# Performance work log

Measured on AMD Instinct MI355X. Metric: run time of the kernel, lower is better.

Reference implementation:

```python
import jax, jax.numpy as jnp
import numpy as np

D_MODEL = 1024
H = 16
D_K = D_MODEL // H
D_FF = 4096
EPS = 1e-6
NEG = -1e9


def setup_inputs() -> dict:
    key = jax.random.key(0)
    ks = jax.random.split(key, 8)
    B, S = 2, 2048
    src = jax.random.normal(ks[0], (B, S, D_MODEL), dtype=jnp.float32)
    src_mask = jnp.ones((B, 1, 1, S), dtype=jnp.int32)
    sc = 1.0 / np.sqrt(D_MODEL)
    wq = jax.random.normal(ks[1], (D_MODEL, D_MODEL), jnp.float32) * sc
    wk = jax.random.normal(ks[2], (D_MODEL, D_MODEL), jnp.float32) * sc
    wv = jax.random.normal(ks[3], (D_MODEL, D_MODEL), jnp.float32) * sc
    wo = jax.random.normal(ks[4], (D_MODEL, D_MODEL), jnp.float32) * sc
    w1 = jax.random.normal(ks[5], (D_FF, D_MODEL), jnp.float32) * sc
    b1 = jnp.zeros((D_FF,), jnp.float32)
    w2 = jax.random.normal(ks[6], (D_MODEL, D_FF), jnp.float32) * (1.0 / np.sqrt(D_FF))
    b2 = jnp.zeros((D_MODEL,), jnp.float32)
    a1 = jnp.ones((1,), jnp.float32)
    be1 = jnp.zeros((1,), jnp.float32)
    a2 = jnp.ones((1,), jnp.float32)
    be2 = jnp.zeros((1,), jnp.float32)
    return dict(src=src, src_mask=src_mask, wq=wq, wk=wk, wv=wv, wo=wo,
                w1=w1, b1=b1, w2=w2, b2=b2, a1=a1, be1=be1, a2=a2, be2=be2)


def layer_norm(x, alpha, bias):
    # torch: mean + unbiased std (ddof=1), eps added to std
    mean = jnp.mean(x, axis=-1, keepdims=True)
    std = jnp.sqrt(jnp.var(x, axis=-1, keepdims=True, ddof=1))
    return alpha * (x - mean) / (std + EPS) + bias


def mha(x, mask, wq, wk, wv, wo):
    B, S, _ = x.shape
    def split(t):  # [B,S,D] -> [B,H,S,D_K]
        return t.reshape(B, S, H, D_K).transpose(0, 2, 1, 3)
    q = split(x @ wq.T)
    k = split(x @ wk.T)
    v = split(x @ wv.T)
    scores = jnp.einsum('bhqd,bhkd->bhqk', q, k) / np.sqrt(D_K)
    scores = jnp.where(mask == 0, NEG, scores)
    attn = jax.nn.softmax(scores, axis=-1)
    out = jnp.einsum('bhqk,bhkd->bhqd', attn, v)
    out = out.transpose(0, 2, 1, 3).reshape(B, S, D_MODEL)
    return out @ wo.T


def reference(src, src_mask, wq, wk, wv, wo, w1, b1, w2, b2, a1, be1, a2, be2):
    x = layer_norm(src, a1, be1)
    src = src + mha(x, src_mask, wq, wk, wv, wo)
    x = layer_norm(src, a2, be2)
    ff = jax.nn.relu(x @ w1.T + b1) @ w2.T + b2
    return src + ff
```

## Files before the change

kernel.cpp:

```cpp
#include <hip/hip_runtime.h>
#include <hip/hip_bf16.h>

typedef unsigned short u16;
typedef unsigned int u32;
typedef float floatx4 __attribute__((ext_vector_type(4)));
typedef __bf16 bf16x8 __attribute__((ext_vector_type(8)));
typedef u16 ushort4v __attribute__((ext_vector_type(4)));
typedef u16 ushort8v __attribute__((ext_vector_type(8)));
typedef u32 u32x2 __attribute__((ext_vector_type(2)));

#define DEVI static __device__ __forceinline__

DEVI u16 f2bf(float f) {
    u32 u = __builtin_bit_cast(u32, f);
    u += 0x7fffu + ((u >> 16) & 1u);
    return (u16)(u >> 16);
}
DEVI float bf2f(u16 h) { return __builtin_bit_cast(float, (u32)h << 16); }

DEVI float fexp2(float x) { return __builtin_amdgcn_exp2f(x); }

DEVI u32 cvtpk_bf16(float lo, float hi) {
    u32 r;
    asm("v_cvt_pk_bf16_f32 %0, %1, %2" : "=v"(r) : "v"(lo), "v"(hi));
    return r;
}

DEVI void async_cp16(const u16* g, u16* l) {
    __builtin_amdgcn_global_load_lds((const __attribute__((address_space(1))) u32*)g,
                                     (__attribute__((address_space(3))) u32*)l, 16, 0, 0);
}

template<int N> DEVI void wait_vmcnt() {
    if constexpr (N == 0)      asm volatile("s_waitcnt vmcnt(0)" ::: "memory");
    else if constexpr (N == 2) asm volatile("s_waitcnt vmcnt(2)" ::: "memory");
    else if constexpr (N == 3) asm volatile("s_waitcnt vmcnt(3)" ::: "memory");
    else if constexpr (N == 4) asm volatile("s_waitcnt vmcnt(4)" ::: "memory");
    else if constexpr (N == 6) asm volatile("s_waitcnt vmcnt(6)" ::: "memory");
    else static_assert(N == 0, "add vmcnt case");
}

#define PH_BAR() asm volatile("s_barrier" ::: "memory")

template<int BM, int BN, int RW, int CW, bool QKV3, int NSPLIT, bool XSWZ,
         bool BIAS, bool RELU, bool RESID, bool OBF16, bool VTW>
__global__ __launch_bounds__(256) void gemm_nt(
    const u16* __restrict__ A,
    const u16* __restrict__ W0, const u16* __restrict__ W1, const u16* __restrict__ W2,
    const float* __restrict__ bias, const float* __restrict__ resid,
    void* __restrict__ o0, void* __restrict__ o1, void* __restrict__ o2,
    void* __restrict__ o3, int K, int lda, int Nper, int NX)
{
    static_assert(RW * CW == 4, "4 waves");
    constexpr int WM = BM / RW, WN = BN / CW;
    constexpr int MI = WM / 16, NI = WN / 16;
    constexpr int LPT = BM / 64 + BN / 64;
    constexpr int ASZ = 3 * BM * 32;
    constexpr int BSZ = 3 * BN * 32;
    __shared__ __align__(16) u16 smem[ASZ + BSZ];
    u16* Asm = smem;
    u16* Bsm = smem + ASZ;
    const int tid = threadIdx.x;
    const int w = tid >> 6, lane = tid & 63;
    const int q = lane >> 4, ml = lane & 15;
    const int wr = w / CW, wc = w % CW;
    int bx = blockIdx.x, by = blockIdx.y;
    if (XSWZ) {
        const int gx = gridDim.x, gy = gridDim.y;
        int L = by * gx + bx;
        int xcd = L & 7, s = L >> 3;
        int mb = gy >> 3;
        by = xcd * mb + s % mb;
        bx = s / mb;
    }
    const int m0 = by * BM;
    size_t kbase = 0;
    const u16* W = W0;
    void* outp = o0;
    if (NSPLIT > 1) {
        int part = bx / NX; bx -= part * NX; kbase = (size_t)part * K;
        outp = (part == 0) ? o0 : (part == 1 ? o1 : (part == 2 ? o2 : o3));
    }
    int n0 = bx * BN;
    bool vwrite = false;
    if (QKV3) {
        int sel = n0 / Nper;
        n0 -= sel * Nper;
        W = (sel == 0) ? W0 : (sel == 1 ? W1 : W2);
        outp = (sel == 0) ? o0 : (sel == 1 ? o1 : o2);
        if (VTW) vwrite = (sel == 2);
    }

    auto stage = [&](int buf, int kt) {
#pragma unroll
        for (int p = 0; p < BM / 64; ++p) {
            int g = p * 256 + tid;
            int r = g >> 2, s = g & 3;
            int c = s ^ ((r >> 1) & 3);
            async_cp16(A + (size_t)(m0 + r) * lda + kbase + kt + c * 8,
                       &Asm[buf * (BM * 32) + (p * 256 + w * 64) * 8]);
        }
#pragma unroll
        for (int p = 0; p < BN / 64; ++p) {
            int g = p * 256 + tid;
            int r = g >> 2, s = g & 3;
            int c = s ^ ((r >> 1) & 3);
            async_cp16(W + (size_t)(n0 + r) * lda + kbase + kt + c * 8,
                       &Bsm[buf * (BN * 32) + (p * 256 + w * 64) * 8]);
        }
    };

    const floatx4 fzero = {0.f, 0.f, 0.f, 0.f};
    floatx4 acc[MI][NI];
#pragma unroll
    for (int i = 0; i < MI; ++i)
#pragma unroll
        for (int j = 0; j < NI; ++j) acc[i][j] = fzero;

    const int nt = K >> 5;
    stage(0, 0);
    stage(1, 32);
    int cb = 0, nb = 2;
    for (int it = 0, kt = 0; it < nt; ++it, kt += 32) {
        wait_vmcnt<LPT>();
        __builtin_amdgcn_s_barrier();
        __builtin_amdgcn_sched_barrier(0);
        int ktn = kt + 64; if (ktn > K - 32) ktn = K - 32;
        stage(nb, ktn);
        __builtin_amdgcn_sched_barrier(0);
        const u16* Asb = &Asm[cb * (BM * 32)];
        const u16* Bsb = &Bsm[cb * (BN * 32)];
        bf16x8 af[MI], bfr[NI];
#pragma unroll
        for (int i = 0; i < MI; ++i) {
            int rm = wr * WM + i * 16 + ml;
            int s = q ^ ((rm >> 1) & 3);
            af[i] = *(const bf16x8*)&Asb[(rm * 4 + s) * 8];
        }
#pragma unroll
        for (int j = 0; j < NI; ++j) {
            int rn = wc * WN + j * 16 + ml;
            int s = q ^ ((rn >> 1) & 3);
            bfr[j] = *(const bf16x8*)&Bsb[(rn * 4 + s) * 8];
        }
#pragma unroll
        for (int i = 0; i < MI; ++i)
#pragma unroll
            for (int j = 0; j < NI; ++j)
                acc[i][j] = __builtin_amdgcn_mfma_f32_16x16x32_bf16(af[i], bfr[j], acc[i][j], 0, 0, 0);
        cb = cb == 2 ? 0 : cb + 1;
        nb = nb == 2 ? 0 : nb + 1;
    }

    wait_vmcnt<0>();

    if constexpr (OBF16) {
        __builtin_amdgcn_s_barrier();
        char* T = (char*)smem;
        if (VTW && vwrite) {
#pragma unroll
            for (int j = 0; j < NI; ++j) {
                int nl = wc * WN + j * 16 + ml;
#pragma unroll
                for (int i = 0; i < MI; ++i) {
                    int m4 = wr * WM + i * 16 + q * 4;
                    u32x2 pk = {(u32)f2bf(acc[i][j][0]) | ((u32)f2bf(acc[i][j][1]) << 16),
                                (u32)f2bf(acc[i][j][2]) | ((u32)f2bf(acc[i][j][3]) << 16)};
                    *(u32x2*)(T + nl * (BM * 2) + ((m4 * 2) ^ ((nl & 15) << 4))) = pk;
                }
            }
            __syncthreads();
            const int bb = m0 >> 11, sres = m0 & 2047;
            constexpr int CPR = BM / 8, RPP = 256 / CPR;
#pragma unroll
            for (int p = 0; p < BN / RPP; ++p) {
                int nr = p * RPP + (tid / CPR);
                int c0 = (tid % CPR) * 8;
                bf16x8 vv = *(const bf16x8*)(T + nr * (BM * 2) + ((c0 * 2) ^ ((nr & 15) << 4)));
                *(bf16x8*)&((u16*)o3)[(size_t)(bb * 1024 + n0 + nr) * 2048 + sres + c0] = vv;
            }
        } else {
#pragma unroll
            for (int j = 0; j < NI; ++j) {
                int col = wc * WN + j * 16 + ml;
                float bj = 0.f;
                if (BIAS) bj = bias[n0 + col];
#pragma unroll
                for (int i = 0; i < MI; ++i) {
#pragma unroll
                    for (int r = 0; r < 4; ++r) {
                        int row = wr * WM + i * 16 + q * 4 + r;
                        float v = acc[i][j][r] + bj;
                        if (RELU) v = fmaxf(v, 0.f);
                        *(u16*)(T + row * (BN * 2) + ((col * 2) ^ ((row & 15) << 4))) = f2bf(v);
                    }
                }
            }
            __syncthreads();
            constexpr int CPR = BN / 8, RPP = 256 / CPR;
#pragma unroll
            for (int p = 0; p < BM / RPP; ++p) {
                int rr = p * RPP + (tid / CPR);
                int c0 = (tid % CPR) * 8;
                bf16x8 vv = *(const bf16x8*)(T + rr * (BN * 2) + ((c0 * 2) ^ ((rr & 15) << 4)));
                *(bf16x8*)&((u16*)outp)[(size_t)(m0 + rr) * Nper + n0 + c0] = vv;
            }
        }
    } else {
#pragma unroll
        for (int j = 0; j < NI; ++j) {
            int gn = n0 + wc * WN + j * 16 + ml;
            float bj = 0.f;
            if (BIAS) bj = bias[gn];
#pragma unroll
            for (int i = 0; i < MI; ++i) {
                int gm0 = m0 + wr * WM + i * 16 + q * 4;
#pragma unroll
                for (int r = 0; r < 4; ++r) {
                    size_t idx = (size_t)(gm0 + r) * Nper + gn;
                    float v = acc[i][j][r] + bj;
                    if (RELU) v = fmaxf(v, 0.f);
                    if (RESID) v += resid[idx];
                    ((float*)outp)[idx] = v;
                }
            }
        }
    }
}

template<bool QKV3, int NSPLIT, bool BIAS, bool RELU, bool VTW>
__global__ __launch_bounds__(512, 2) void gemm8p(
    const u16* __restrict__ A,
    const u16* __restrict__ W0, const u16* __restrict__ W1, const u16* __restrict__ W2,
    const float* __restrict__ bias,
    void* __restrict__ o0, void* __restrict__ o1, void* __restrict__ o2,
    void* __restrict__ o3, int K, int lda, int Nper, int NX)
{
    __shared__ __align__(16) u16 smem[65536];
    u16* Asm = smem;
    u16* Bsm = smem + 32768;
    const int tid = threadIdx.x;
    const int w = tid >> 6, lane = tid & 63;
    const int q = lane >> 4, ml = lane & 15;
    const int wr = w >> 2, wc = w & 3;
    int bx = blockIdx.x, by = blockIdx.y;
    {
        const int gx = gridDim.x, gy = gridDim.y;
        int L = by * gx + bx;
        int xcd = L & 7, s = L >> 3;
        int mb = gy >> 3;
        by = xcd * mb + s % mb;
        bx = s / mb;
    }
    const int m0 = by * 256;
    size_t kbase = 0;
    const u16* W = W0;
    void* outp = o0;
    if (NSPLIT > 1) {
        int part = bx / NX; bx -= part * NX; kbase = (size_t)part * K;
        outp = (part == 0) ? o0 : (part == 1 ? o1 : (part == 2 ? o2 : o3));
    }
    int n0 = bx * 256;
    if (QKV3) {
        int sel = n0 / Nper; n0 -= sel * Nper;
        W = (sel == 0) ? W0 : (sel == 1 ? W1 : W2);
        outp = (sel == 0) ? o0 : (sel == 1 ? o1 : o2);
    }

    auto stA = [&](int d, int kh, int kt) {
#pragma unroll
        for (int p = 0; p < 2; ++p) {
            int c = p * 512 + tid;
            int r = c >> 2;
            int sc = (c & 3) ^ ((r >> 1) & 3);
            async_cp16(A + (size_t)(m0 + r) * lda + kbase + kt + kh * 32 + sc * 8,
                       &Asm[(d * 2 + kh) * 8192 + (p * 512 + w * 64) * 8]);
        }
    };
    auto stB = [&](int d, int kh, int kt) {
#pragma unroll
        for (int p = 0; p < 2; ++p) {
            int c = p * 512 + tid;
            int r = c >> 2;
            int sc = (c & 3) ^ ((r >> 1) & 3);
            async_cp16(W + (size_t)(n0 + r) * lda + kbase + kt + kh * 32 + sc * 8,
                       &Bsm[(d * 2 + kh) * 8192 + (p * 512 + w * 64) * 8]);
        }
    };
    auto rdA = [&](int d, int kh, int i) -> bf16x8 {
        int rm = wr * 128 + i * 16 + ml;
        return *(const bf16x8*)&Asm[(d * 2 + kh) * 8192 + (rm * 4 + (q ^ ((rm >> 1) & 3))) * 8];
    };
    auto rdB = [&](int d, int kh, int j) -> bf16x8 {
        int rn = wc * 64 + j * 16 + ml;
        return *(const bf16x8*)&Bsm[(d * 2 + kh) * 8192 + (rn * 4 + (q ^ ((rn >> 1) & 3))) * 8];
    };

    const floatx4 fzero = {0.f, 0.f, 0.f, 0.f};
    floatx4 acc[8][4];
#pragma unroll
    for (int i = 0; i < 8; ++i)
#pragma unroll
        for (int j = 0; j < 4; ++j) acc[i][j] = fzero;

#define PHASE(d, kh, ih, STG, VM)                                              \
    {                                                                          \
        if (ih == 0) {                                                         \
            _Pragma("unroll")                                                  \
            for (int j = 0; j < 4; ++j) bfr[j] = rdB(d, kh, j);                \
        }                                                                      \
        _Pragma("unroll")                                                      \
        for (int ii = 0; ii < 4; ++ii) af[ii] = rdA(d, kh, (ih) * 4 + ii);     \
        STG;                                                                   \
        if (VM) wait_vmcnt<4>();                                               \
        PH_BAR();                                                              \
        __builtin_amdgcn_s_setprio(1);                                         \
        _Pragma("unroll")                                                      \
        for (int ii = 0; ii < 4; ++ii)                                         \
            _Pragma("unroll")                                                  \
            for (int j = 0; j < 4; ++j)                                        \
                acc[(ih) * 4 + ii][j] = __builtin_amdgcn_mfma_f32_16x16x32_bf16( \
                    af[ii], bfr[j], acc[(ih) * 4 + ii][j], 0, 0, 0);           \
        __builtin_amdgcn_s_setprio(0);                                         \
        PH_BAR();                                                              \
    }

    const int R = K >> 7;
    stA(0, 0, 0); stB(0, 0, 0); stA(0, 1, 0); stB(0, 1, 0);
    wait_vmcnt<0>();
    PH_BAR();

    for (int rr = 0; rr < R; ++rr) {
        const int kt1 = rr * 128 + 64;
        const int kt2 = (rr * 128 + 128 <= K - 64) ? rr * 128 + 128 : K - 64;
        bf16x8 af[4], bfr[4];
        PHASE(0, 0, 0, stA(1, 0, kt1), 0)
        PHASE(0, 0, 1, stB(1, 0, kt1), 1)
        PHASE(0, 1, 0, stA(1, 1, kt1), 0)
        PHASE(0, 1, 1, stB(1, 1, kt1), 1)
        PHASE(1, 0, 0, stA(0, 0, kt2), 0)
        PHASE(1, 0, 1, stB(0, 0, kt2), 1)
        PHASE(1, 1, 0, stA(0, 1, kt2), 0)
        PHASE(1, 1, 1, stB(0, 1, kt2), 1)
    }
#undef PHASE
    wait_vmcnt<0>();
    __builtin_amdgcn_s_barrier();

    char* T = (char*)smem;
#pragma unroll
    for (int j = 0; j < 4; ++j) {
        int col = wc * 64 + j * 16 + ml;
        float bj = 0.f;
        if (BIAS) bj = bias[n0 + col];
#pragma unroll
        for (int i = 0; i < 8; ++i) {
#pragma unroll
            for (int r = 0; r < 4; ++r) {
                int row = wr * 128 + i * 16 + q * 4 + r;
                float v = acc[i][j][r] + bj;
                if (RELU) v = fmaxf(v, 0.f);
                *(u16*)(T + row * 512 + ((col * 2) ^ ((row & 15) << 5))) = f2bf(v);
            }
        }
    }
    __syncthreads();
#pragma unroll
    for (int p = 0; p < 16; ++p) {
        int rr = p * 16 + (tid >> 5);
        int c0 = (tid & 31) * 8;
        bf16x8 vv = *(const bf16x8*)(T + rr * 512 + ((c0 * 2) ^ ((rr & 15) << 5)));
        *(bf16x8*)&((u16*)outp)[(size_t)(m0 + rr) * Nper + n0 + c0] = vv;
    }
}

__global__ __launch_bounds__(256, 2) void flash9(
    const u16* __restrict__ Q, const u16* __restrict__ Kg,
    const u16* __restrict__ Vt, const float* __restrict__ biasv,
    u16* __restrict__ O)
{
    __shared__ __align__(16) u16 smem[24576];
    const int tid = threadIdx.x;
    const int w = tid >> 6, lane = tid & 63;
    const int qw = w & 1, kv = w >> 1;
    const int q = lane >> 4, ml = lane & 15;
    int bx = blockIdx.x, by = blockIdx.y;
    {
        int L = by * 16 + bx;
        int xcd = L & 7, s = L >> 3;
        by = xcd * 4 + (s >> 4);
        bx = s & 15;
    }
    const int b = by >> 4, h = by & 15;
    const size_t rowQ = (size_t)(b * 2048 + bx * 128);
    const float KSC = 0.125f * 1.4426950408889634f;
    const floatx4 fzero = {0.f, 0.f, 0.f, 0.f};

    bf16x8 qa[4][2];
#pragma unroll
    for (int qg = 0; qg < 4; ++qg)
#pragma unroll
        for (int c = 0; c < 2; ++c)
            qa[qg][c] = *(const bf16x8*)&Q[(rowQ + qw * 64 + qg * 16 + ml) * 1024
                                           + h * 64 + q * 8 + c * 32];

    auto stage = [&](int buf, int it) {
        {
            int row = tid >> 3, sl = tid & 7;
            int ch = sl ^ ((row & 3) | (((row >> 3) & 1) << 2));
#pragma unroll
            for (int hf = 0; hf < 2; ++hf)
                async_cp16(Kg + (size_t)(b * 2048 + hf * 1024 + it * 32 + row) * 1024
                               + h * 64 + ch * 8,
                           &smem[(hf * 3 + buf) * 2048 + w * 512]);
        }
        {
            int row = tid >> 2, sl = tid & 3;
            int ch = sl ^ ((row >> 1) & 3);
#pragma unroll
            for (int hf = 0; hf < 2; ++hf)
                async_cp16(Vt + (size_t)(b * 1024 + h * 64 + row) * 2048
                               + hf * 1024 + it * 32 + ch * 8,
                           &smem[12288 + (hf * 3 + buf) * 2048 + w * 512]);
        }
    };

    floatx4 oacc[4][4];
    float lsum[4] = {0.f, 0.f, 0.f, 0.f};
#pragma unroll
    for (int qg = 0; qg < 4; ++qg)
#pragma unroll
        for (int d = 0; d < 4; ++d) oacc[qg][d] = fzero;

    const int swk = (ml & 3) | (((ml >> 2) & 1) << 2);
    const int re = ((ml >> 2) << 3) + (ml & 3);

    stage(0, 0);
    stage(1, 1);
    int cb = 0, nb = 2;
    for (int it = 0; it < 32; ++it) {
        asm volatile("s_waitcnt vmcnt(4)" ::: "memory");
        __builtin_amdgcn_s_barrier();
        __builtin_amdgcn_sched_barrier(0);
        const int s0 = kv * 1024 + it * 32;
        const float4 be = *(const float4*)&biasv[b * 2048 + s0 + q * 8];
        const float4 bo = *(const float4*)&biasv[b * 2048 + s0 + q * 8 + 4];
        __builtin_amdgcn_sched_barrier(0);
        stage(nb, it + 2 < 32 ? it + 2 : 31);

        const u16* Kb = &smem[(kv * 3 + cb) * 2048];
        const u16* Vb = &smem[12288 + (kv * 3 + cb) * 2048];

        bf16x8 ke0 = *(const bf16x8*)&Kb[(re + 0) * 64 + ((0 + q) ^ swk) * 8];
        bf16x8 ke1 = *(const bf16x8*)&Kb[(re + 0) * 64 + ((4 + q) ^ swk) * 8];
        bf16x8 ko0 = *(const bf16x8*)&Kb[(re + 4) * 64 + ((0 + q) ^ swk) * 8];
        bf16x8 ko1 = *(const bf16x8*)&Kb[(re + 4) * 64 + ((4 + q) ^ swk) * 8];
        bf16x8 pfrag[4];
#pragma unroll
        for (int qg = 0; qg < 4; ++qg) {
            floatx4 te = fzero, to = fzero;
            te = __builtin_amdgcn_mfma_f32_16x16x32_bf16(ke0, qa[qg][0], te, 0, 0, 0);
            te = __builtin_amdgcn_mfma_f32_16x16x32_bf16(ke1, qa[qg][1], te, 0, 0, 0);
            to = __builtin_amdgcn_mfma_f32_16x16x32_bf16(ko0, qa[qg][0], to, 0, 0, 0);
            to = __builtin_amdgcn_mfma_f32_16x16x32_bf16(ko1, qa[qg][1], to, 0, 0, 0);
            float pe0 = fexp2(fmaf(te[0], KSC, be.x));
            float pe1 = fexp2(fmaf(te[1], KSC, be.y));
            float pe2 = fexp2(fmaf(te[2], KSC, be.z));
            float pe3 = fexp2(fmaf(te[3], KSC, be.w));
            float po0 = fexp2(fmaf(to[0], KSC, bo.x));
            float po1 = fexp2(fmaf(to[1], KSC, bo.y));
            float po2 = fexp2(fmaf(to[2], KSC, bo.z));
            float po3 = fexp2(fmaf(to[3], KSC, bo.w));
            lsum[qg] += ((pe0 + pe1) + (pe2 + pe3)) + ((po0 + po1) + (po2 + po3));
            u32 pk[4];
            pk[0] = cvtpk_bf16(pe0, pe1);
            pk[1] = cvtpk_bf16(pe2, pe3);
            pk[2] = cvtpk_bf16(po0, po1);
            pk[3] = cvtpk_bf16(po2, po3);
            pfrag[qg] = __builtin_bit_cast(bf16x8, *(uint4*)pk);
        }
#pragma unroll
        for (int dt = 0; dt < 4; ++dt) {
            int vrow = dt * 16 + ml;
            bf16x8 vf = *(const bf16x8*)&Vb[vrow * 32 + ((q ^ ((vrow >> 1) & 3)) * 8)];
#pragma unroll
            for (int qg = 0; qg < 4; ++qg)
                oacc[qg][dt] = __builtin_amdgcn_mfma_f32_16x16x32_bf16(
                    vf, pfrag[qg], oacc[qg][dt], 0, 0, 0);
        }
        cb = cb == 2 ? 0 : cb + 1;
        nb = nb == 2 ? 0 : nb + 1;
    }

    __syncthreads();
    float* sO = (float*)smem;
    float* sL = (float*)smem + 8192;
    if (kv == 1) {
#pragma unroll
        for (int qg = 0; qg < 4; ++qg) {
            sL[(qw * 4 + qg) * 64 + lane] = lsum[qg];
#pragma unroll
            for (int dt = 0; dt < 4; ++dt)
                *(floatx4*)&sO[((qw * 4 + qg) * 4 + dt) * 256 + lane * 4] = oacc[qg][dt];
        }
    }
    __syncthreads();
    if (kv == 1) return;
#pragma unroll
    for (int qg = 0; qg < 4; ++qg) {
        lsum[qg] += sL[(qw * 4 + qg) * 64 + lane];
#pragma unroll
        for (int dt = 0; dt < 4; ++dt)
            oacc[qg][dt] += *(const floatx4*)&sO[((qw * 4 + qg) * 4 + dt) * 256 + lane * 4];
        float ls = lsum[qg];
        ls += __shfl_xor(ls, 16, 64);
        ls += __shfl_xor(ls, 32, 64);
        const float rcp = 1.f / ls;
        const size_t row = rowQ + qw * 64 + qg * 16 + ml;
#pragma unroll
        for (int dt = 0; dt < 4; ++dt)
#pragma unroll
            for (int rp = 0; rp < 4; rp += 2) {
                u32 pk = (u32)f2bf(oacc[qg][dt][rp] * rcp)
                       | ((u32)f2bf(oacc[qg][dt][rp + 1] * rcp) << 16);
                *(u32*)&O[row * 1024 + h * 64 + dt * 16 + q * 4 + rp] = pk;
            }
    }
}

DEVI void ln_row(const float* __restrict__ x, float ga, float gb,
                 u16* __restrict__ y, int row, int tid)
{
    const float4 v = ((const float4*)(x + (size_t)row * 1024))[tid];
    float s = v.x + v.y + v.z + v.w;
    float ss = v.x * v.x + v.y * v.y + v.z * v.z + v.w * v.w;
#pragma unroll
    for (int d = 1; d < 64; d <<= 1) { s += __shfl_xor(s, d, 64); ss += __shfl_xor(ss, d, 64); }
    __shared__ float ps[4], pss[4];
    const int w = tid >> 6, lane = tid & 63;
    if (lane == 0) { ps[w] = s; pss[w] = ss; }
    __syncthreads();
    s = ps[0] + ps[1] + ps[2] + ps[3];
    ss = pss[0] + pss[1] + pss[2] + pss[3];
    float mean = s * (1.f / 1024.f);
    float var = fmaxf((ss - s * mean) * (1.f / 1023.f), 0.f);
    float sc = ga / (sqrtf(var) + 1e-6f);
    ushort4v o;
    o[0] = f2bf((v.x - mean) * sc + gb);
    o[1] = f2bf((v.y - mean) * sc + gb);
    o[2] = f2bf((v.z - mean) * sc + gb);
    o[3] = f2bf((v.w - mean) * sc + gb);
    ((ushort4v*)(y + (size_t)row * 1024))[tid] = o;
}

__global__ __launch_bounds__(256) void ln_bf16(const float* __restrict__ x,
    const float* __restrict__ ga, const float* __restrict__ gb, u16* __restrict__ y)
{
    ln_row(x, ga[0], gb[0], y, blockIdx.x, threadIdx.x);
}

__global__ __launch_bounds__(256) void prep(
    const float* __restrict__ wq, const float* __restrict__ wk,
    const float* __restrict__ wv, const float* __restrict__ wo,
    const float* __restrict__ w1, const float* __restrict__ w2,
    u16* __restrict__ wqb, u16* __restrict__ wkb, u16* __restrict__ wvb,
    u16* __restrict__ wob, u16* __restrict__ w1b, u16* __restrict__ w2b,
    const int* __restrict__ m, float* __restrict__ biasv,
    const float* __restrict__ src, const float* __restrict__ a1,
    const float* __restrict__ be1, u16* __restrict__ xln1)
{
    const int bx = blockIdx.x;
    if (bx < 12288) {
        size_t i = (size_t)bx * 256 + threadIdx.x;
        const float* s; u16* d; size_t off;
        if (i < 262144)       { s = wq; d = wqb; off = i; }
        else if (i < 524288)  { s = wk; d = wkb; off = i - 262144; }
        else if (i < 786432)  { s = wv; d = wvb; off = i - 524288; }
        else if (i < 1048576) { s = wo; d = wob; off = i - 786432; }
        else if (i < 2097152) { s = w1; d = w1b; off = i - 1048576; }
        else                  { s = w2; d = w2b; off = i - 2097152; }
        float4 v = ((const float4*)s)[off];
        ushort4v o = {f2bf(v.x), f2bf(v.y), f2bf(v.z), f2bf(v.w)};
        ((ushort4v*)d)[off] = o;
    } else if (bx < 12304) {
        int i = (bx - 12288) * 256 + threadIdx.x;
        biasv[i] = m[i] ? 0.f : -1.442695e9f;
    } else {
        ln_row(src, a1[0], be1[0], xln1, bx - 12304, threadIdx.x);
    }
}

__global__ __launch_bounds__(256) void ff2_fin(
    const u16* __restrict__ p0, const u16* __restrict__ p1,
    const u16* __restrict__ p2, const u16* __restrict__ p3,
    const float* __restrict__ b2, const float* __restrict__ resid,
    float* __restrict__ out)
{
    const size_t i = (size_t)blockIdx.x * 256 + threadIdx.x;
    ushort4v a = *(const ushort4v*)&p0[i * 4];
    ushort4v b = *(const ushort4v*)&p1[i * 4];
    ushort4v c = *(const ushort4v*)&p2[i * 4];
    ushort4v d = *(const ushort4v*)&p3[i * 4];
    float4 r = ((const float4*)resid)[i];
    float4 bb = ((const float4*)b2)[i & 255];
    float4 o;
    o.x = ((bf2f(a[0]) + bf2f(b[0])) + (bf2f(c[0]) + bf2f(d[0]))) + r.x + bb.x;
    o.y = ((bf2f(a[1]) + bf2f(b[1])) + (bf2f(c[1]) + bf2f(d[1]))) + r.y + bb.y;
    o.z = ((bf2f(a[2]) + bf2f(b[2])) + (bf2f(c[2]) + bf2f(d[2]))) + r.z + bb.z;
    o.w = ((bf2f(a[3]) + bf2f(b[3])) + (bf2f(c[3]) + bf2f(d[3]))) + r.w + bb.w;
    ((float4*)out)[i] = o;
}

extern "C" void kernel_launch(void* const* d_in, const int* in_sizes, int n_in,
                              void* d_out, int out_size, void* d_ws, size_t ws_size,
                              hipStream_t stream)
{
    const float* src = (const float*)d_in[0];
    const int* msk   = (const int*)d_in[1];
    const float* wq  = (const float*)d_in[2];
    const float* wk  = (const float*)d_in[3];
    const float* wv  = (const float*)d_in[4];
    const float* wo  = (const float*)d_in[5];
    const float* w1  = (const float*)d_in[6];
    const float* b1  = (const float*)d_in[7];
    const float* w2  = (const float*)d_in[8];
    const float* b2  = (const float*)d_in[9];
    const float* a1  = (const float*)d_in[10];
    const float* be1 = (const float*)d_in[11];
    const float* a2  = (const float*)d_in[12];
    const float* be2 = (const float*)d_in[13];
    float* out = (float*)d_out;

    char* ws = (char*)d_ws;
    const size_t MB = (size_t)1 << 20;
    u16* wqb  = (u16*)(ws + 0 * MB);
    u16* wkb  = (u16*)(ws + 2 * MB);
    u16* wvb  = (u16*)(ws + 4 * MB);
    u16* wob  = (u16*)(ws + 6 * MB);
    u16* w1b  = (u16*)(ws + 8 * MB);
    u16* w2b  = (u16*)(ws + 16 * MB);
    u16* xln1 = (u16*)(ws + 24 * MB);
    u16* attn = xln1;
    u16* Qb   = (u16*)(ws + 32 * MB);
    u16* xln2 = Qb;
    u16* Kb   = (u16*)(ws + 40 * MB);
    u16* Vt   = (u16*)(ws + 56 * MB);
    float* biasv = (float*)(ws + 64 * MB);
    u16* h1   = (u16*)(ws + 40 * MB);
    float* src2 = (float*)(ws + 72 * MB);
    u16* P0 = (u16*)(ws + 0 * MB);
    u16* P1 = (u16*)(ws + 8 * MB);
    u16* P2 = (u16*)(ws + 24 * MB);
    u16* P3 = (u16*)(ws + 32 * MB);

    prep<<<16400, 256, 0, stream>>>(wq, wk, wv, wo, w1, w2,
                                    wqb, wkb, wvb, wob, w1b, w2b,
                                    msk, biasv, src, a1, be1, xln1);

    gemm_nt<128, 128, 2, 2, true, 1, true, false, false, false, true, true><<<dim3(24, 32), 256, 0, stream>>>(
        xln1, wqb, wkb, wvb, nullptr, nullptr, Qb, Kb, nullptr, Vt, 1024, 1024, 1024, 0);

    flash9<<<dim3(16, 32), 256, 0, stream>>>(Qb, Kb, Vt, biasv, attn);

    gemm_nt<128, 64, 4, 1, false, 1, true, false, false, true, false, false><<<dim3(16, 32), 256, 0, stream>>>(
        attn, wob, nullptr, nullptr, nullptr, src, src2, nullptr, nullptr, nullptr,
        1024, 1024, 1024, 0);

    ln_bf16<<<4096, 256, 0, stream>>>(src2, a2, be2, xln2);

    gemm8p<false, 1, true, true, false><<<dim3(16, 16), 512, 0, stream>>>(
        xln2, w1b, nullptr, nullptr, b1, h1, nullptr, nullptr, nullptr,
        1024, 1024, 4096, 0);

    gemm8p<false, 4, false, false, false><<<dim3(16, 16), 512, 0, stream>>>(
        h1, w2b, nullptr, nullptr, nullptr, P0, P1, P2, P3,
        1024, 4096, 1024, 4);

    ff2_fin<<<4096, 256, 0, stream>>>(P0, P1, P2, P3, b2, src2, out);
}
```

Measured before the change: 314.9 us.

## Compute softmax row sums via MFMA with ones vector and 2D XCD swizzle

The attention kernel now takes the softmax denominator from an extra MFMA that multiplies the bf16 probability fragment by a ones vector. This replaces eight VALU adds per query group and the cross-lane shuffle reduction at the end, and it makes the denominator use the same bf16-rounded probabilities as the PV product. Separately, the GEMM block swizzle is changed from a 1D split of M rows per XCD to a 2D 4x2 grouping over M and N. The aim is better L2 reuse of both the A and W tiles on each XCD, at the cost of extra matrix-core work in attention.

```diff
diff --git a/kernel.cpp b/kernel.cpp
--- a/kernel.cpp
+++ b/kernel.cpp
@@ -41,6 +41,15 @@
 }
 
 #define PH_BAR() asm volatile("s_barrier" ::: "memory")
+
+DEVI void xcd_swizzle(int& bx, int& by, int gx, int gy) {
+    int L = by * gx + bx;
+    int xcd = L & 7, s = L >> 3;
+    int gh = gy >> 2, xh = gx >> 1;
+    int mg = xcd & 3, ng = xcd >> 2;
+    by = mg * gh + s % gh;
+    bx = ng * xh + s / gh;
+}
 
 template<int BM, int BN, int RW, int CW, bool QKV3, int NSPLIT, bool XSWZ,
          bool BIAS, bool RELU, bool RESID, bool OBF16, bool VTW>
@@ -65,14 +74,7 @@
     const int q = lane >> 4, ml = lane & 15;
     const int wr = w / CW, wc = w % CW;
     int bx = blockIdx.x, by = blockIdx.y;
-    if (XSWZ) {
-        const int gx = gridDim.x, gy = gridDim.y;
-        int L = by * gx + bx;
-        int xcd = L & 7, s = L >> 3;
-        int mb = gy >> 3;
-        by = xcd * mb + s % mb;
-        bx = s / mb;
-    }
+    if (XSWZ) xcd_swizzle(bx, by, gridDim.x, gridDim.y);
     const int m0 = by * BM;
     size_t kbase = 0;
     const u16* W = W0;
@@ -244,14 +246,7 @@
     const int q = lane >> 4, ml = lane & 15;
     const int wr = w >> 2, wc = w & 3;
     int bx = blockIdx.x, by = blockIdx.y;
-    {
-        const int gx = gridDim.x, gy = gridDim.y;
-        int L = by * gx + bx;
-        int xcd = L & 7, s = L >> 3;
-        int mb = gy >> 3;
-        by = xcd * mb + s % mb;
-        bx = s / mb;
-    }
+    xcd_swizzle(bx, by, gridDim.x, gridDim.y);
     const int m0 = by * 256;
     size_t kbase = 0;
     const u16* W = W0;
@@ -395,6 +390,9 @@
     const size_t rowQ = (size_t)(b * 2048 + bx * 128);
     const float KSC = 0.125f * 1.4426950408889634f;
     const floatx4 fzero = {0.f, 0.f, 0.f, 0.f};
+    const ushort8v onesv = {0x3F80, 0x3F80, 0x3F80, 0x3F80,
+                            0x3F80, 0x3F80, 0x3F80, 0x3F80};
+    const bf16x8 vone = __builtin_bit_cast(bf16x8, onesv);
 
     bf16x8 qa[4][2];
 #pragma unroll
@@ -426,11 +424,13 @@
     };
 
     floatx4 oacc[4][4];
-    float lsum[4] = {0.f, 0.f, 0.f, 0.f};
-#pragma unroll
-    for (int qg = 0; qg < 4; ++qg)
+    floatx4 lacc[4];
+#pragma unroll
+    for (int qg = 0; qg < 4; ++qg) {
+        lacc[qg] = fzero;
 #pragma unroll
         for (int d = 0; d < 4; ++d) oacc[qg][d] = fzero;
+    }
 
     const int swk = (ml & 3) | (((ml >> 2) & 1) << 2);
     const int re = ((ml >> 2) << 3) + (ml & 3);
@@ -471,13 +471,14 @@
             float po1 = fexp2(fmaf(to[1], KSC, bo.y));
             float po2 = fexp2(fmaf(to[2], KSC, bo.z));
             float po3 = fexp2(fmaf(to[3], KSC, bo.w));
-            lsum[qg] += ((pe0 + pe1) + (pe2 + pe3)) + ((po0 + po1) + (po2 + po3));
             u32 pk[4];
             pk[0] = cvtpk_bf16(pe0, pe1);
             pk[1] = cvtpk_bf16(pe2, pe3);
             pk[2] = cvtpk_bf16(po0, po1);
             pk[3] = cvtpk_bf16(po2, po3);
             pfrag[qg] = __builtin_bit_cast(bf16x8, *(uint4*)pk);
+            lacc[qg] = __builtin_amdgcn_mfma_f32_16x16x32_bf16(
+                vone, pfrag[qg], lacc[qg], 0, 0, 0);
         }
 #pragma unroll
         for (int dt = 0; dt < 4; ++dt) {
@@ -498,7 +499,7 @@
     if (kv == 1) {
 #pragma unroll
         for (int qg = 0; qg < 4; ++qg) {
-            sL[(qw * 4 + qg) * 64 + lane] = lsum[qg];
+            sL[(qw * 4 + qg) * 64 + lane] = lacc[qg][0];
 #pragma unroll
             for (int dt = 0; dt < 4; ++dt)
                 *(floatx4*)&sO[((qw * 4 + qg) * 4 + dt) * 256 + lane * 4] = oacc[qg][dt];
@@ -508,13 +509,10 @@
     if (kv == 1) return;
 #pragma unroll
     for (int qg = 0; qg < 4; ++qg) {
-        lsum[qg] += sL[(qw * 4 + qg) * 64 + lane];
+        float ls = lacc[qg][0] + sL[(qw * 4 + qg) * 64 + lane];
 #pragma unroll
         for (int dt = 0; dt < 4; ++dt)
             oacc[qg][dt] += *(const floatx4*)&sO[((qw * 4 + qg) * 4 + dt) * 256 + lane * 4];
-        float ls = lsum[qg];
-        ls += __shfl_xor(ls, 16, 64);
-        ls += __shfl_xor(ls, 32, 64);
         const float rcp = 1.f / ls;
         const size_t row = rowQ + qw * 64 + qg * 16 + ml;
 #pragma unroll
```

Measured after the change: 316.3 us. No clear change (+0.4%).
